# Kernel tuning notes

Hardware: AMD Instinct MI355X
Metric: run time of the kernel (lower is better)

## Reference

```python
import jax, jax.numpy as jnp
import numpy as np

N0, C1, C2 = 100000, 10000, 1000
E0 = 1_600_000
IN = 128
H = 128
OUT = 128


def _pool_edges(ei, ew, cluster, C):
    # PyG pool_edge: remap via cluster, drop self loops, coalesce (sum weights)
    m = cluster[ei]
    mask = m[0] != m[1]
    m = m[:, mask]
    w = ew[mask]
    keys = m[0] * C + m[1]
    uk, inv = np.unique(keys, return_inverse=True)
    w2 = np.bincount(inv, weights=w).astype(np.float32)
    return np.stack([uk // C, uk % C]).astype(np.int64), w2


def _with_self_loops(ei, ew, N):
    # gcn_norm(add_remaining_self_loops, fill_value=1); base edges have no loops
    row = np.concatenate([ei[0], np.arange(N)]).astype(np.int64)
    col = np.concatenate([ei[1], np.arange(N)]).astype(np.int64)
    w = np.concatenate([ew, np.ones(N, np.float32)])
    return row, col, w


def setup_inputs() -> dict:
    rng = np.random.default_rng(0)
    ei = rng.integers(0, N0, size=(2, E0))
    ei = ei[:, ei[0] != ei[1]]
    ew = np.ones(ei.shape[1], np.float32)
    # guaranteed-surjective cluster assignments (stand-in for Louvain output)
    c1 = rng.permutation(np.arange(N0) % C1).astype(np.int64)
    c2 = rng.permutation(np.arange(C1) % C2).astype(np.int64)
    ei1, ew1 = _pool_edges(ei, ew, c1, C1)
    ei2, ew2 = _pool_edges(ei1, ew1, c2, C2)
    r0, co0, w0 = _with_self_loops(ei, ew, N0)
    r1, co1, w1 = _with_self_loops(ei1, ew1, C1)
    r2, co2, w2 = _with_self_loops(ei2, ew2, C2)

    key = jax.random.key(0)
    ks = jax.random.split(key, 16)
    def lin(k, fi, fo):
        return jax.random.normal(k, (fi, fo), jnp.float32) / np.sqrt(fi)
    inp = {
        'x': jax.random.normal(ks[0], (N0, IN), jnp.float32),
        'W_pre': lin(ks[1], IN, H), 'b_pre': jnp.zeros((H,), jnp.float32),
        'W_u0': lin(ks[2], H, H), 'b_u0': jnp.zeros((H,), jnp.float32),
        'W_u1': lin(ks[3], H, H), 'b_u1': jnp.zeros((H,), jnp.float32),
        'W_u2': lin(ks[4], H, H), 'b_u2': jnp.zeros((H,), jnp.float32),
        'W_d0': lin(ks[5], H, OUT), 'b_d0': jnp.zeros((OUT,), jnp.float32),
        'W_d1': lin(ks[6], H, H), 'b_d1': jnp.zeros((H,), jnp.float32),
        'row0': jnp.asarray(r0), 'col0': jnp.asarray(co0), 'ew0': jnp.asarray(w0),
        'row1': jnp.asarray(r1), 'col1': jnp.asarray(co1), 'ew1': jnp.asarray(w1),
        'row2': jnp.asarray(r2), 'col2': jnp.asarray(co2), 'ew2': jnp.asarray(w2),
        'cluster1': jnp.asarray(c1), 'cluster2': jnp.asarray(c2),
    }
    return inp


def _gcn(x, W, b, row, col, ew, N):
    # PyG GCNConv: sym-normalized aggregation at target (col)
    deg = jax.ops.segment_sum(ew, col, num_segments=N)
    dinv = jnp.where(deg > 0, jax.lax.rsqrt(deg), 0.0)
    norm = dinv[row] * ew * dinv[col]
    h = x @ W                                   # [N, F_out]
    out = jax.ops.segment_sum(h[row] * norm[:, None], col, num_segments=N)
    return out + b


def _seg_mean(x, cluster, C):
    s = jax.ops.segment_sum(x, cluster, num_segments=C)
    cnt = jax.ops.segment_sum(jnp.ones((x.shape[0], 1), x.dtype), cluster,
                              num_segments=C)
    return s / jnp.maximum(cnt, 1.0)


def reference(x, W_pre, b_pre, W_u0, b_u0, W_u1, b_u1, W_u2, b_u2,
              W_d0, b_d0, W_d1, b_d1,
              row0, col0, ew0, row1, col1, ew1, row2, col2, ew2,
              cluster1, cluster2):
    # --- up (coarsening) path ---
    h = x @ W_pre + b_pre                                   # preembed
    x0 = jax.nn.relu(_gcn(h, W_u0, b_u0, row0, col0, ew0, N0))
    x1 = _seg_mean(x0, cluster1, C1)                        # avg_pool level 1
    x1 = jax.nn.relu(_gcn(x1, W_u1, b_u1, row1, col1, ew1, C1))
    x2 = _seg_mean(x1, cluster2, C2)                        # avg_pool level 2
    x2 = jax.nn.relu(_gcn(x2, W_u2, b_u2, row2, col2, ew2, C2))
    # --- down (unpooling) path; down convs use all-ones edge weights ---
    y = x1 + x2[cluster2]
    y = jax.nn.relu(_gcn(y, W_d1, b_d1, row1, col1, jnp.ones_like(ew1), C1))
    y = x0 + y[cluster1]
    y = _gcn(y, W_d0, b_d0, row0, col0, jnp.ones_like(ew0), N0)
    return y
```

## Files before the change

kernel.cpp:

```cpp
#include <hip/hip_runtime.h>

#define HH 128
static constexpr int kN0 = 100000;
static constexpr int kC1 = 10000;
static constexpr int kC2 = 1000;

static constexpr int B0 = kN0;
static constexpr int B1 = B0 + kC1;
static constexpr int B2 = B1 + kC2;
static constexpr int B3 = B2 + kC1;
static constexpr int NTOT = B3 + kC2;

static constexpr int NB0 = (kN0 + 127) / 128;
static constexpr int NB1 = (kC1 + 7) / 8;
static constexpr int NB2 = kC2;
static constexpr int NBP1 = (kC1 + 127) / 128;
static constexpr int NBP2 = (kC2 + 15) / 16;
static constexpr int Q0 = NB0;
static constexpr int Q1 = Q0 + NB1;
static constexpr int Q2 = Q1 + NB2;
static constexpr int Q3 = Q2 + NBP1;
static constexpr int NBK = Q3 + NBP2;

__device__ __forceinline__ int bucket_of(int bin) {
  if (bin < B0) return bin >> 7;
  if (bin < B1) return Q0 + ((bin - B0) >> 3);
  if (bin < B2) return Q1 + (bin - B1);
  if (bin < B3) return Q2 + ((bin - B2) >> 7);
  return Q3 + ((bin - B3) >> 4);
}

__device__ __forceinline__ unsigned int f2_to_bf2(float a, float b) {
  unsigned int ua = __float_as_uint(a);
  unsigned int ub = __float_as_uint(b);
  ua = (ua + 0x7fffu + ((ua >> 16) & 1u)) >> 16;
  ub = (ub + 0x7fffu + ((ub >> 16) & 1u)) & 0xffff0000u;
  return ua | ub;
}
__device__ __forceinline__ unsigned short f2bf(float f) {
  unsigned int u = __float_as_uint(f);
  u = (u + 0x7fffu + ((u >> 16) & 1u)) >> 16;
  return (unsigned short)u;
}
__device__ __forceinline__ float bf2f(unsigned short s) {
  return __uint_as_float(((unsigned int)s) << 16);
}

using bf16x8 = __attribute__((ext_vector_type(8))) short;
using f32x4 = __attribute__((ext_vector_type(4))) float;

__global__ __launch_bounds__(256) void p1_kernel(const int* __restrict__ col0,
                                                 const int* __restrict__ col1,
                                                 const int* __restrict__ col2,
                                                 const int* __restrict__ cl1,
                                                 const int* __restrict__ cl2,
                                                 int E0, int E1, int E2,
                                                 int* __restrict__ bucketCnt) {
  __shared__ int h[NBK];
  for (int i = threadIdx.x; i < NBK; i += 256) h[i] = 0;
  __syncthreads();
  int T0 = E0, T1 = T0 + E1, T2 = T1 + E2, T3 = T2 + kN0, T4 = T3 + kC1;
  for (int g = blockIdx.x * 256 + threadIdx.x; g < T4; g += gridDim.x * 256) {
    int bin;
    if (g < T0)      bin = col0[g];
    else if (g < T1) bin = B0 + col1[g - T0];
    else if (g < T2) bin = B1 + col2[g - T1];
    else if (g < T3) bin = B2 + cl1[g - T2];
    else             bin = B3 + cl2[g - T3];
    atomicAdd(&h[bucket_of(bin)], 1);
  }
  __syncthreads();
  for (int i = threadIdx.x; i < NBK; i += 256) {
    int c = h[i];
    if (c) atomicAdd(&bucketCnt[i], c);
  }
}

__global__ __launch_bounds__(1024) void p2_kernel(const int* __restrict__ bucketCnt,
                                                  int* __restrict__ bucketStart,
                                                  int* __restrict__ cursor,
                                                  int* __restrict__ startsg, int T) {
  int t = threadIdx.x;
  int v[4]; int s = 0;
#pragma unroll
  for (int j = 0; j < 4; j++) {
    int i = t * 4 + j;
    v[j] = (i < NBK) ? bucketCnt[i] : 0;
    s += v[j];
  }
  int lane = t & 63, w = t >> 6;
  int incl = s;
  for (int o = 1; o < 64; o <<= 1) { int u = __shfl_up(incl, o); if (lane >= o) incl += u; }
  __shared__ int wt[16];
  if (lane == 63) wt[w] = incl;
  __syncthreads();
  if (t == 0) { int run = 0; for (int i = 0; i < 16; i++) { int c = wt[i]; wt[i] = run; run += c; } }
  __syncthreads();
  int ex = wt[w] + incl - s;
#pragma unroll
  for (int j = 0; j < 4; j++) {
    int i = t * 4 + j;
    if (i < NBK) { bucketStart[i] = ex; cursor[i] = ex; }
    ex += v[j];
  }
  if (t == 0) { bucketStart[NBK] = T; startsg[NTOT] = T; }
}

__global__ __launch_bounds__(256) void p3_kernel(const int* __restrict__ col0,
                                                 const int* __restrict__ col1,
                                                 const int* __restrict__ col2,
                                                 const int* __restrict__ cl1,
                                                 const int* __restrict__ cl2,
                                                 const int* __restrict__ row0,
                                                 const int* __restrict__ row1,
                                                 const int* __restrict__ row2,
                                                 const float* __restrict__ ew1,
                                                 const float* __restrict__ ew2,
                                                 int E0, int E1, int E2,
                                                 int* __restrict__ cursor,
                                                 int4* __restrict__ part) {
  __shared__ int h[NBK];
  __shared__ int gbase[NBK];
  for (int i = threadIdx.x; i < NBK; i += 256) h[i] = 0;
  __syncthreads();
  int T0 = E0, T1 = T0 + E1, T2 = T1 + E2, T3 = T2 + kN0, T4 = T3 + kC1;
  int base = blockIdx.x * 4096;
  int bins[16], srcs[16], rk[16];
  float wv[16];
#pragma unroll
  for (int j = 0; j < 16; j++) {
    int g = base + threadIdx.x + j * 256;
    int bin = -1, src = 0; float w = 0.f;
    if (g < T4) {
      if (g < T0) { bin = col0[g]; src = row0[g]; }
      else if (g < T1) { int e = g - T0; bin = B0 + col1[e]; src = row1[e]; w = ew1[e]; }
      else if (g < T2) { int e = g - T1; bin = B1 + col2[e]; src = row2[e]; w = ew2[e]; }
      else if (g < T3) { int e = g - T2; bin = B2 + cl1[e]; src = e; }
      else             { int e = g - T3; bin = B3 + cl2[e]; src = e; }
    }
    bins[j] = bin; srcs[j] = src; wv[j] = w;
    rk[j] = (bin >= 0) ? atomicAdd(&h[bucket_of(bin)], 1) : 0;
  }
  __syncthreads();
  for (int i = threadIdx.x; i < NBK; i += 256) {
    int c = h[i];
    gbase[i] = c ? atomicAdd(&cursor[i], c) : 0;
  }
  __syncthreads();
#pragma unroll
  for (int j = 0; j < 16; j++) {
    if (bins[j] >= 0) {
      int slot = gbase[bucket_of(bins[j])] + rk[j];
      part[slot] = make_int4(bins[j], srcs[j], __float_as_int(wv[j]), 0);
    }
  }
}

__global__ __launch_bounds__(256) void p4_kernel(const int* __restrict__ bucketStart,
                                                 const int4* __restrict__ part,
                                                 int* __restrict__ startsg,
                                                 int* __restrict__ rowS,
                                                 float* __restrict__ ewSm) {
  int b = blockIdx.x;
  int binLo, width;
  if (b < Q0)      { binLo = b << 7;                 width = 128; if (binLo + width > B0) width = B0 - binLo; }
  else if (b < Q1) { binLo = B0 + ((b - Q0) << 3);   width = 8; }
  else if (b < Q2) { binLo = B1 + (b - Q1);          width = 1; }
  else if (b < Q3) { binLo = B2 + ((b - Q2) << 7);   width = 128; if (binLo + width > B3) width = B3 - binLo; }
  else             { binLo = B3 + ((b - Q3) << 4);   width = 16; if (binLo + width > NTOT) width = NTOT - binLo; }
  int base = bucketStart[b], nend = bucketStart[b + 1];
  int t = threadIdx.x;

  if (width == 1) {
    if (t == 0) startsg[binLo] = base;
    bool isEw = (binLo >= B0 && binLo < B2);
    for (int i = base + t; i < nend; i += 256) {
      int4 it = part[i];
      rowS[i] = it.y;
      if (isEw) ewSm[i] = __int_as_float(it.z);
    }
    return;
  }

  __shared__ int h[128];
  __shared__ int cur[128];
  if (t < 128) h[t] = 0;
  __syncthreads();
  for (int i = base + t; i < nend; i += 256) atomicAdd(&h[part[i].x - binLo], 1);
  __syncthreads();
  if (t == 0) {
    int run = 0;
    for (int j = 0; j < width; j++) {
      cur[j] = run;
      startsg[binLo + j] = base + run;
      run += h[j];
    }
  }
  __syncthreads();
  for (int i = base + t; i < nend; i += 256) {
    int4 it = part[i];
    int k = it.x;
    int r = atomicAdd(&cur[k - binLo], 1);
    int dst = base + r;
    rowS[dst] = it.y;
    if (k >= B0 && k < B2) ewSm[dst] = __int_as_float(it.z);
  }
}

__global__ void dinv_kernel(const int* __restrict__ startsg, const float* __restrict__ ewSm,
                            float* __restrict__ d0, float* __restrict__ d1w,
                            float* __restrict__ d1o, float* __restrict__ d2) {
  int t = blockIdx.x * 256 + threadIdx.x;
  if (t < kN0) {
    int c = startsg[t + 1] - startsg[t];
    d0[t] = c > 0 ? rsqrtf((float)c) : 0.f;
  }
  int wid = t >> 6, lane = t & 63;
  if (wid < kC1) {
    int s = startsg[B0 + wid], e = startsg[B0 + wid + 1];
    float a = 0.f;
    for (int k = s + lane; k < e; k += 64) a += ewSm[k];
    for (int o = 32; o > 0; o >>= 1) a += __shfl_down(a, o);
    if (lane == 0) {
      d1w[wid] = a > 0.f ? rsqrtf(a) : 0.f;
      int c = e - s;
      d1o[wid] = c > 0 ? rsqrtf((float)c) : 0.f;
    }
  } else if (wid < kC1 + kC2) {
    int w2 = wid - kC1;
    int s = startsg[B1 + w2], e = startsg[B1 + w2 + 1];
    float a = 0.f;
    for (int k = s + lane; k < e; k += 64) a += ewSm[k];
    for (int o = 32; o > 0; o >>= 1) a += __shfl_down(a, o);
    if (lane == 0) d2[w2] = a > 0.f ? rsqrtf(a) : 0.f;
  }
}

__global__ void wprep_kernel(const int* __restrict__ rowS, const float* __restrict__ ewSm,
                             const float* __restrict__ d1w, const float* __restrict__ d2,
                             int E0, int E1, int E2,
                             float* __restrict__ wAll) {
  int e = blockIdx.x * 256 + threadIdx.x + E0;
  int tot = E0 + E1 + E2;
  if (e >= tot) return;
  int r = rowS[e];
  if (e < E0 + E1) {
    wAll[e] = d1w[r] * ewSm[e];
  } else {
    wAll[e] = d2[r] * ewSm[e];
  }
}

__global__ __launch_bounds__(256) void matmul_kernel(const float* __restrict__ X,
                                                     const float* __restrict__ Xadd,
                                                     const int* __restrict__ cl,
                                                     const float* __restrict__ W,
                                                     const float* __restrict__ bias,
                                                     const float* __restrict__ rowScale,
                                                     float* __restrict__ Y,
                                                     unsigned int* __restrict__ Ybf, int N) {
  __shared__ float Ws[64 * 128];
  __shared__ float Xs[32 * 128];
  int t = threadIdx.x;
  int rbase = blockIdx.x * 32;
  const float4* X4 = (const float4*)X;
  float4* Xs4 = (float4*)Xs;
#pragma unroll
  for (int i = 0; i < 4; i++) {
    int idx = t + 256 * i;
    int fr = idx >> 5, fc = idx & 31;
    int row = rbase + fr; if (row >= N) row = N - 1;
    float4 v = X4[(size_t)row * 32 + fc];
    if (Xadd) {
      int c = cl[row];
      float4 u = ((const float4*)Xadd)[(size_t)c * 32 + fc];
      v.x += u.x; v.y += u.y; v.z += u.z; v.w += u.w;
    }
    Xs4[idx] = v;
  }
  float acc[4][4];
#pragma unroll
  for (int r = 0; r < 4; r++)
#pragma unroll
    for (int cc = 0; cc < 4; cc++) acc[r][cc] = 0.f;
  int c0 = (t & 31) * 4;
  int rl = (t >> 5) * 4;
  const float4* W4 = (const float4*)W;
  float4* Ws4 = (float4*)Ws;
  for (int half = 0; half < 2; half++) {
    __syncthreads();
#pragma unroll
    for (int i = 0; i < 8; i++) {
      int idx = t + 256 * i;
      Ws4[idx] = W4[half * 2048 + idx];
    }
    __syncthreads();
#pragma unroll 4
    for (int k = 0; k < 64; k++) {
      float4 w4 = *(const float4*)(Ws + k * 128 + c0);
      float xv[4];
#pragma unroll
      for (int r = 0; r < 4; r++) xv[r] = Xs[(rl + r) * 128 + half * 64 + k];
#pragma unroll
      for (int r = 0; r < 4; r++) {
        acc[r][0] = fmaf(xv[r], w4.x, acc[r][0]);
        acc[r][1] = fmaf(xv[r], w4.y, acc[r][1]);
        acc[r][2] = fmaf(xv[r], w4.z, acc[r][2]);
        acc[r][3] = fmaf(xv[r], w4.w, acc[r][3]);
      }
    }
  }
  float4 b4 = make_float4(0.f, 0.f, 0.f, 0.f);
  if (bias) b4 = *(const float4*)(bias + c0);
#pragma unroll
  for (int r = 0; r < 4; r++) {
    int row = rbase + rl + r;
    if (row < N) {
      float sc = rowScale ? rowScale[row] : 1.f;
      float4 o;
      o.x = (acc[r][0] + b4.x) * sc; o.y = (acc[r][1] + b4.y) * sc;
      o.z = (acc[r][2] + b4.z) * sc; o.w = (acc[r][3] + b4.w) * sc;
      if (Ybf) {
        unsigned int pk0 = f2_to_bf2(o.x, o.y);
        unsigned int pk1 = f2_to_bf2(o.z, o.w);
        *(uint2*)(Ybf + (size_t)row * 64 + (c0 >> 1)) = make_uint2(pk0, pk1);
      } else {
        *(float4*)(Y + (size_t)row * 128 + c0) = o;
      }
    }
  }
}

__global__ __launch_bounds__(256, 2) void mfma_gemm_kernel(
    const float* __restrict__ X, const float* __restrict__ Xadd,
    const int* __restrict__ cl, const float* __restrict__ W,
    const float* __restrict__ bias, const float* __restrict__ rowScale,
    unsigned int* __restrict__ Ybf, int N) {
  __shared__ unsigned int Bt[128 * 64];
  int t = threadIdx.x;
  {
    int n = t & 127, kh = t >> 7;
#pragma unroll
    for (int k = kh * 64; k < kh * 64 + 64; k += 2) {
      float a = W[(size_t)k * 128 + n];
      float b = W[(size_t)(k + 1) * 128 + n];
      unsigned int pk = (unsigned int)f2bf(a) | ((unsigned int)f2bf(b) << 16);
      unsigned int byteoff = ((unsigned int)(n * 256 + k * 2)) ^ (((unsigned int)n & 7u) << 4);
      *(unsigned int*)((char*)Bt + byteoff) = pk;
    }
  }
  __syncthreads();
  int wv = t >> 6, lane = t & 63;
  int g = lane >> 4, mrow = lane & 15;
  int rbase = blockIdx.x * 128 + wv * 32;
  bf16x8 ahi[2][4], alo[2][4];
#pragma unroll
  for (int mt = 0; mt < 2; mt++) {
    int row = rbase + mt * 16 + mrow;
    int rc = row < N ? row : N - 1;
    const float4* Xr = (const float4*)(X + (size_t)rc * 128);
    const float4* Ar = Xadd ? (const float4*)(Xadd + (size_t)cl[rc] * 128) : nullptr;
#pragma unroll
    for (int ks = 0; ks < 4; ks++) {
      int c4 = ks * 8 + g * 2;
      float4 v0 = Xr[c4], v1 = Xr[c4 + 1];
      if (Ar) {
        float4 u0 = Ar[c4], u1 = Ar[c4 + 1];
        v0.x += u0.x; v0.y += u0.y; v0.z += u0.z; v0.w += u0.w;
        v1.x += u1.x; v1.y += u1.y; v1.z += u1.z; v1.w += u1.w;
      }
      float vv[8] = {v0.x, v0.y, v0.z, v0.w, v1.x, v1.y, v1.z, v1.w};
      bf16x8 h, l;
#pragma unroll
      for (int j = 0; j < 8; j++) {
        unsigned short hb = f2bf(vv[j]);
        h[j] = (short)hb;
        l[j] = (short)f2bf(vv[j] - bf2f(hb));
      }
      ahi[mt][ks] = h; alo[mt][ks] = l;
    }
  }
  f32x4 acc[2][8];
#pragma unroll
  for (int mt = 0; mt < 2; mt++)
#pragma unroll
    for (int nt = 0; nt < 8; nt++) acc[mt][nt] = (f32x4){0.f, 0.f, 0.f, 0.f};
#pragma unroll
  for (int ks = 0; ks < 4; ks++) {
#pragma unroll
    for (int nt = 0; nt < 8; nt++) {
      int n = nt * 16 + mrow;
      unsigned int byteoff =
          ((unsigned int)(n * 256 + ks * 64 + g * 16)) ^ (((unsigned int)n & 7u) << 4);
      bf16x8 b = *(const bf16x8*)((const char*)Bt + byteoff);
      acc[0][nt] = __builtin_amdgcn_mfma_f32_16x16x32_bf16(ahi[0][ks], b, acc[0][nt], 0, 0, 0);
      acc[1][nt] = __builtin_amdgcn_mfma_f32_16x16x32_bf16(ahi[1][ks], b, acc[1][nt], 0, 0, 0);
      acc[0][nt] = __builtin_amdgcn_mfma_f32_16x16x32_bf16(alo[0][ks], b, acc[0][nt], 0, 0, 0);
      acc[1][nt] = __builtin_amdgcn_mfma_f32_16x16x32_bf16(alo[1][ks], b, acc[1][nt], 0, 0, 0);
    }
  }
#pragma unroll
  for (int mt = 0; mt < 2; mt++) {
#pragma unroll
    for (int r = 0; r < 4; r++) {
      int row = rbase + mt * 16 + g * 4 + r;
      if (row < N) {
        float sc = rowScale ? rowScale[row] : 1.f;
#pragma unroll
        for (int nt = 0; nt < 4; nt++) {
          int c = nt * 16 + mrow;
          float lo = (acc[mt][nt][r] + (bias ? bias[c] : 0.f)) * sc;
          float hi = (acc[mt][nt + 4][r] + (bias ? bias[c + 64] : 0.f)) * sc;
          Ybf[(size_t)row * 64 + c] = (unsigned int)f2bf(lo) | ((unsigned int)f2bf(hi) << 16);
        }
      }
    }
  }
}

__global__ __launch_bounds__(256) void agg_kernel(const unsigned int* __restrict__ Hf,
                                                  float* __restrict__ out,
                                                  const int* __restrict__ starts,
                                                  const int* __restrict__ rowS,
                                                  const float* __restrict__ dinv,
                                                  const float* __restrict__ bias,
                                                  int C, int relu) {
  int wid = (blockIdx.x * blockDim.x + threadIdx.x) >> 6;
  int lane = threadIdx.x & 63;
  if (wid >= C) return;
  int h = lane >> 5, hl = lane & 31;
  const uint2* Hf2 = (const uint2*)Hf;
  int s = starts[wid], e = starts[wid + 1];
  float dc = dinv[wid];
  float a0 = 0.f, a1 = 0.f, b0 = 0.f, b1 = 0.f;
  for (int base = s; base < e; base += 64) {
    int n = e - base; if (n > 64) n = 64;
    int r = rowS[base + (lane < n ? lane : 0)];
    for (int j = 0; j < n; j += 16) {
#pragma unroll
      for (int u = 0; u < 8; u++) {
        int eidx = j + u * 2 + h;
        bool v = eidx < n;
        int rr = __shfl(r, v ? eidx : 0);
        uint2 pv = Hf2[(size_t)rr * 32 + hl];
        if (!v) { pv.x = 0u; pv.y = 0u; }
        a0 += __uint_as_float(pv.x << 16);
        b0 += __uint_as_float(pv.x & 0xffff0000u);
        a1 += __uint_as_float(pv.y << 16);
        b1 += __uint_as_float(pv.y & 0xffff0000u);
      }
    }
  }
  a0 += __shfl_xor(a0, 32); a1 += __shfl_xor(a1, 32);
  b0 += __shfl_xor(b0, 32); b1 += __shfl_xor(b1, 32);
  int c0 = h * 64 + hl * 2;
  float o0 = (h ? b0 : a0) * dc + bias[c0];
  float o1 = (h ? b1 : a1) * dc + bias[c0 + 1];
  if (relu) { o0 = fmaxf(o0, 0.f); o1 = fmaxf(o1, 0.f); }
  *(float2*)(out + (size_t)wid * 128 + c0) = make_float2(o0, o1);
}

__global__ __launch_bounds__(256) void aggb_kernel(const unsigned int* __restrict__ Hf,
                                                   float* __restrict__ out,
                                                   const int* __restrict__ starts,
                                                   const int* __restrict__ rowS,
                                                   const float* __restrict__ wS,
                                                   const float* __restrict__ dinv,
                                                   const float* __restrict__ bias,
                                                   int C, int relu) {
  int node = blockIdx.x;
  if (node >= C) return;
  int wv = threadIdx.x >> 6, lane = threadIdx.x & 63;
  int h = lane >> 5, hl = lane & 31;
  const uint2* Hf2 = (const uint2*)Hf;
  int s = starts[node], e = starts[node + 1];
  float a0 = 0.f, a1 = 0.f, a2 = 0.f, a3 = 0.f;
  for (int base = s + wv * 64; base < e; base += 256) {
    int n = e - base; if (n > 64) n = 64;
    int moff = base + (lane < n ? lane : 0);
    int r = rowS[moff];
    float w = wS[moff];
    for (int j = 0; j < n; j += 16) {
#pragma unroll
      for (int u = 0; u < 8; u++) {
        int eidx = j + u * 2 + h;
        bool v = eidx < n;
        int rr = __shfl(r, v ? eidx : 0);
        float ww = __shfl(w, v ? eidx : 0);
        if (!v) ww = 0.f;
        uint2 pv = Hf2[(size_t)rr * 32 + hl];
        a0 = fmaf(ww, __uint_as_float(pv.x << 16), a0);
        a1 = fmaf(ww, __uint_as_float(pv.x & 0xffff0000u), a1);
        a2 = fmaf(ww, __uint_as_float(pv.y << 16), a2);
        a3 = fmaf(ww, __uint_as_float(pv.y & 0xffff0000u), a3);
      }
    }
  }
  a0 += __shfl_xor(a0, 32); a1 += __shfl_xor(a1, 32);
  a2 += __shfl_xor(a2, 32); a3 += __shfl_xor(a3, 32);
  __shared__ float4 sh[4][32];
  if (h == 0) sh[wv][hl] = make_float4(a0, a1, a2, a3);
  __syncthreads();
  if (threadIdx.x < 32) {
    float4 v0 = sh[0][threadIdx.x], v1 = sh[1][threadIdx.x];
    float4 v2 = sh[2][threadIdx.x], v3 = sh[3][threadIdx.x];
    float dc = dinv[node];
    int c0 = threadIdx.x * 4;
    float4 bb = *(const float4*)(bias + c0);
    float4 o;
    o.x = (v0.x + v1.x + v2.x + v3.x) * dc + bb.x;
    o.y = (v0.y + v1.y + v2.y + v3.y) * dc + bb.y;
    o.z = (v0.z + v1.z + v2.z + v3.z) * dc + bb.z;
    o.w = (v0.w + v1.w + v2.w + v3.w) * dc + bb.w;
    if (relu) {
      o.x = fmaxf(o.x, 0.f); o.y = fmaxf(o.y, 0.f);
      o.z = fmaxf(o.z, 0.f); o.w = fmaxf(o.w, 0.f);
    }
    *(float4*)(out + (size_t)node * 128 + c0) = o;
  }
}

__global__ __launch_bounds__(256) void aggb1_kernel(const unsigned int* __restrict__ Hf,
                                                    float* __restrict__ out,
                                                    const int* __restrict__ starts,
                                                    const int* __restrict__ rowS,
                                                    const float* __restrict__ dinv,
                                                    const float* __restrict__ bias,
                                                    int C, int relu) {
  int node = blockIdx.x;
  if (node >= C) return;
  int wv = threadIdx.x >> 6, lane = threadIdx.x & 63;
  int h = lane >> 5, hl = lane & 31;
  const uint2* Hf2 = (const uint2*)Hf;
  int s = starts[node], e = starts[node + 1];
  float a0 = 0.f, a1 = 0.f, a2 = 0.f, a3 = 0.f;
  for (int base = s + wv * 64; base < e; base += 256) {
    int n = e - base; if (n > 64) n = 64;
    int r = rowS[base + (lane < n ? lane : 0)];
    for (int j = 0; j < n; j += 16) {
#pragma unroll
      for (int u = 0; u < 8; u++) {
        int eidx = j + u * 2 + h;
        bool v = eidx < n;
        int rr = __shfl(r, v ? eidx : 0);
        uint2 pv = Hf2[(size_t)rr * 32 + hl];
        if (!v) { pv.x = 0u; pv.y = 0u; }
        a0 += __uint_as_float(pv.x << 16);
        a1 += __uint_as_float(pv.x & 0xffff0000u);
        a2 += __uint_as_float(pv.y << 16);
        a3 += __uint_as_float(pv.y & 0xffff0000u);
      }
    }
  }
  a0 += __shfl_xor(a0, 32); a1 += __shfl_xor(a1, 32);
  a2 += __shfl_xor(a2, 32); a3 += __shfl_xor(a3, 32);
  __shared__ float4 sh[4][32];
  if (h == 0) sh[wv][hl] = make_float4(a0, a1, a2, a3);
  __syncthreads();
  if (threadIdx.x < 32) {
    float4 v0 = sh[0][threadIdx.x], v1 = sh[1][threadIdx.x];
    float4 v2 = sh[2][threadIdx.x], v3 = sh[3][threadIdx.x];
    float dc = dinv[node];
    int c0 = threadIdx.x * 4;
    float4 bb = *(const float4*)(bias + c0);
    float4 o;
    o.x = (v0.x + v1.x + v2.x + v3.x) * dc + bb.x;
    o.y = (v0.y + v1.y + v2.y + v3.y) * dc + bb.y;
    o.z = (v0.z + v1.z + v2.z + v3.z) * dc + bb.z;
    o.w = (v0.w + v1.w + v2.w + v3.w) * dc + bb.w;
    if (relu) {
      o.x = fmaxf(o.x, 0.f); o.y = fmaxf(o.y, 0.f);
      o.z = fmaxf(o.z, 0.f); o.w = fmaxf(o.w, 0.f);
    }
    *(float4*)(out + (size_t)node * 128 + c0) = o;
  }
}

__global__ __launch_bounds__(256) void pool_kernel(const float* __restrict__ src,
                                                   float* __restrict__ out,
                                                   const int* __restrict__ starts,
                                                   const int* __restrict__ rowS, int C) {
  int wid = (blockIdx.x * blockDim.x + threadIdx.x) >> 6;
  int lane = threadIdx.x & 63;
  if (wid >= C) return;
  int s = starts[wid], e = starts[wid + 1];
  float ax0 = 0.f, ay0 = 0.f, ax1 = 0.f, ay1 = 0.f;
  int m = s;
  for (; m + 7 < e; m += 8) {
    int idx[8];
#pragma unroll
    for (int u = 0; u < 8; u++) idx[u] = rowS[m + u];
#pragma unroll
    for (int u = 0; u < 8; u++) {
      float2 v = *(const float2*)(src + (size_t)idx[u] * 128 + lane * 2);
      if (u & 1) { ax1 += v.x; ay1 += v.y; } else { ax0 += v.x; ay0 += v.y; }
    }
  }
  for (; m < e; m++) {
    int id = rowS[m];
    const float2 v = *(const float2*)(src + (size_t)id * 128 + lane * 2);
    ax0 += v.x; ay0 += v.y;
  }
  float inv = (e > s) ? 1.f / (float)(e - s) : 0.f;
  *(float2*)(out + (size_t)wid * 128 + lane * 2) =
      make_float2((ax0 + ax1) * inv, (ay0 + ay1) * inv);
}


extern "C" void kernel_launch(void* const* d_in, const int* in_sizes, int n_in,
                              void* d_out, int out_size, void* d_ws, size_t ws_size,
                              hipStream_t stream) {
  const float* x     = (const float*)d_in[0];
  const float* W_pre = (const float*)d_in[1];
  const float* b_pre = (const float*)d_in[2];
  const float* W_u0  = (const float*)d_in[3];
  const float* b_u0  = (const float*)d_in[4];
  const float* W_u1  = (const float*)d_in[5];
  const float* b_u1  = (const float*)d_in[6];
  const float* W_u2  = (const float*)d_in[7];
  const float* b_u2  = (const float*)d_in[8];
  const float* W_d0  = (const float*)d_in[9];
  const float* b_d0  = (const float*)d_in[10];
  const float* W_d1  = (const float*)d_in[11];
  const float* b_d1  = (const float*)d_in[12];
  const int* row0 = (const int*)d_in[13];
  const int* col0 = (const int*)d_in[14];
  const int* row1 = (const int*)d_in[16];
  const int* col1 = (const int*)d_in[17];
  const float* ew1 = (const float*)d_in[18];
  const int* row2 = (const int*)d_in[19];
  const int* col2 = (const int*)d_in[20];
  const float* ew2 = (const float*)d_in[21];
  const int* cluster1 = (const int*)d_in[22];
  const int* cluster2 = (const int*)d_in[23];
  int E0 = in_sizes[13], E1 = in_sizes[16], E2 = in_sizes[19];
  float* out = (float*)d_out;
  int Ttot = E0 + E1 + E2 + kN0 + kC1;
  int Etot = E0 + E1 + E2;

  char* basep = (char*)d_ws;
  size_t off = 0;
  auto alloc = [&](size_t bytes) -> char* {
    char* p = basep + off;
    off = (off + bytes + 255) & ~(size_t)255;
    return p;
  };
  int* bucketCnt = (int*)alloc((size_t)NBK * 4);
  size_t zero_bytes = off;
  int* bucketStart = (int*)alloc((size_t)(NBK + 1) * 4);
  int* cursor      = (int*)alloc((size_t)NBK * 4);
  int* startsg     = (int*)alloc((size_t)(NTOT + 1) * 4);
  int* rowS  = (int*)alloc((size_t)Ttot * 4);
  float* ewS = (float*)alloc((size_t)(E1 + E2) * 4);
  float* ewSm = ewS - E0;
  float* dinv0  = (float*)alloc((size_t)kN0 * 4);
  float* dinv1w = (float*)alloc((size_t)kC1 * 4);
  float* dinv1o = (float*)alloc((size_t)kC1 * 4);
  float* dinv2  = (float*)alloc((size_t)kC2 * 4);
  size_t watermark = off;
  int4* part = (int4*)alloc((size_t)Ttot * 16);
  off = watermark;
  float* wAll = (float*)alloc((size_t)Etot * 4);
  float* Wf   = (float*)alloc((size_t)128 * 128 * 4);
  float* bfv  = (float*)alloc((size_t)128 * 4);
  float* A    = (float*)alloc((size_t)kN0 * HH * 4);
  float* s1a  = (float*)alloc((size_t)kC1 * HH * 4);
  float* s1b  = (float*)alloc((size_t)kC1 * HH * 4);
  float* s2a  = (float*)alloc((size_t)kC2 * HH * 4);
  unsigned int* s1bb = (unsigned int*)alloc((size_t)kC1 * 64 * 4);
  unsigned int* s2bb = (unsigned int*)alloc((size_t)kC2 * 64 * 4);
  unsigned int* s1cb = (unsigned int*)alloc((size_t)kC1 * 64 * 4);
  unsigned int* tb   = (unsigned int*)alloc((size_t)kN0 * 64 * 4);
  unsigned int* t0   = (unsigned int*)d_out;

  hipMemsetAsync(d_ws, 0, zero_bytes, stream);

  auto cdiv = [](int a, int b) { return (a + b - 1) / b; };

  p1_kernel<<<256, 256, 0, stream>>>(col0, col1, col2, cluster1, cluster2, E0, E1, E2, bucketCnt);
  p2_kernel<<<1, 1024, 0, stream>>>(bucketCnt, bucketStart, cursor, startsg, Ttot);
  p3_kernel<<<cdiv(Ttot, 4096), 256, 0, stream>>>(col0, col1, col2, cluster1, cluster2,
                                                  row0, row1, row2, ew1, ew2, E0, E1, E2,
                                                  cursor, part);
  p4_kernel<<<NBK, 256, 0, stream>>>(bucketStart, part, startsg, rowS, ewSm);
  dinv_kernel<<<cdiv((kC1 + kC2) * 64, 256), 256, 0, stream>>>(startsg, ewSm, dinv0, dinv1w,
                                                               dinv1o, dinv2);
  wprep_kernel<<<cdiv(E1 + E2, 256), 256, 0, stream>>>(rowS, ewSm, dinv1w, dinv2,
                                                       E0, E1, E2, wAll);

  matmul_kernel<<<cdiv(128, 32), 256, 0, stream>>>(W_pre, nullptr, nullptr, W_u0, nullptr,
                                                   nullptr, Wf, nullptr, 128);
  matmul_kernel<<<1, 256, 0, stream>>>(b_pre, nullptr, nullptr, W_u0, nullptr,
                                       nullptr, bfv, nullptr, 1);
  mfma_gemm_kernel<<<cdiv(kN0, 128), 256, 0, stream>>>(x, nullptr, nullptr, Wf, bfv, dinv0,
                                                       t0, kN0);
  agg_kernel<<<cdiv(kN0, 4), 256, 0, stream>>>(t0, A, startsg, rowS, dinv0, b_u0, kN0, 1);
  pool_kernel<<<cdiv(kC1, 4), 256, 0, stream>>>(A, s1a, startsg + B2, rowS, kC1);
  matmul_kernel<<<cdiv(kC1, 32), 256, 0, stream>>>(s1a, nullptr, nullptr, W_u1, nullptr,
                                                   nullptr, nullptr, s1bb, kC1);
  aggb_kernel<<<kC1, 256, 0, stream>>>(s1bb, s1a, startsg + B0, rowS, wAll, dinv1w, b_u1, kC1, 1);
  pool_kernel<<<cdiv(kC2, 4), 256, 0, stream>>>(s1a, s2a, startsg + B3, rowS, kC2);
  matmul_kernel<<<cdiv(kC2, 32), 256, 0, stream>>>(s2a, nullptr, nullptr, W_u2, nullptr,
                                                   nullptr, nullptr, s2bb, kC2);
  aggb_kernel<<<kC2, 256, 0, stream>>>(s2bb, s2a, startsg + B1, rowS, wAll, dinv2, b_u2, kC2, 1);
  matmul_kernel<<<cdiv(kC1, 32), 256, 0, stream>>>(s1a, s2a, cluster2, W_d1, nullptr,
                                                   dinv1o, nullptr, s1cb, kC1);
  aggb1_kernel<<<kC1, 256, 0, stream>>>(s1cb, s1b, startsg + B0, rowS, dinv1o, b_d1, kC1, 1);
  mfma_gemm_kernel<<<cdiv(kN0, 128), 256, 0, stream>>>(A, s1b, cluster1, W_d0, nullptr, dinv0,
                                                       tb, kN0);
  agg_kernel<<<cdiv(kN0, 4), 256, 0, stream>>>(tb, out, startsg, rowS, dinv0, b_d0, kN0, 0);
}
```

Measured before the change: 634.6 us.

## Partition scatter kernel with few large chunks and two-pass histogram

The bucket-scatter kernel now launches 128 blocks, each covering a large contiguous chunk of edges, in place of one block per 4096 edges. Each block makes a histogram pass over its chunk, reserves global ranges once per bucket, then re-reads the edges and scatters using shared-memory atomics as local cursors. This cuts the number of global cursor atomics and per-block bucket reservations, at the cost of reading the column arrays twice and running far fewer blocks. Slots within a bucket are now assigned in nondeterministic order within each block.

```diff
diff --git a/kernel.cpp b/kernel.cpp
--- a/kernel.cpp
+++ b/kernel.cpp
@@ -21,6 +21,8 @@
 static constexpr int Q2 = Q1 + NB2;
 static constexpr int Q3 = Q2 + NBP1;
 static constexpr int NBK = Q3 + NBP2;
+
+static constexpr int P3_BLOCKS = 128;
 
 __device__ __forceinline__ int bucket_of(int bin) {
   if (bin < B0) return bin >> 7;
@@ -120,39 +122,36 @@
                                                  int* __restrict__ cursor,
                                                  int4* __restrict__ part) {
   __shared__ int h[NBK];
-  __shared__ int gbase[NBK];
   for (int i = threadIdx.x; i < NBK; i += 256) h[i] = 0;
   __syncthreads();
   int T0 = E0, T1 = T0 + E1, T2 = T1 + E2, T3 = T2 + kN0, T4 = T3 + kC1;
-  int base = blockIdx.x * 4096;
-  int bins[16], srcs[16], rk[16];
-  float wv[16];
-#pragma unroll
-  for (int j = 0; j < 16; j++) {
-    int g = base + threadIdx.x + j * 256;
-    int bin = -1, src = 0; float w = 0.f;
-    if (g < T4) {
-      if (g < T0) { bin = col0[g]; src = row0[g]; }
-      else if (g < T1) { int e = g - T0; bin = B0 + col1[e]; src = row1[e]; w = ew1[e]; }
-      else if (g < T2) { int e = g - T1; bin = B1 + col2[e]; src = row2[e]; w = ew2[e]; }
-      else if (g < T3) { int e = g - T2; bin = B2 + cl1[e]; src = e; }
-      else             { int e = g - T3; bin = B3 + cl2[e]; src = e; }
-    }
-    bins[j] = bin; srcs[j] = src; wv[j] = w;
-    rk[j] = (bin >= 0) ? atomicAdd(&h[bucket_of(bin)], 1) : 0;
+  int chunk = ((T4 + P3_BLOCKS - 1) / P3_BLOCKS + 255) & ~255;
+  int start = blockIdx.x * chunk;
+  int end = start + chunk; if (end > T4) end = T4;
+  for (int g = start + (int)threadIdx.x; g < end; g += 256) {
+    int bin;
+    if (g < T0)      bin = col0[g];
+    else if (g < T1) bin = B0 + col1[g - T0];
+    else if (g < T2) bin = B1 + col2[g - T1];
+    else if (g < T3) bin = B2 + cl1[g - T2];
+    else             bin = B3 + cl2[g - T3];
+    atomicAdd(&h[bucket_of(bin)], 1);
   }
   __syncthreads();
   for (int i = threadIdx.x; i < NBK; i += 256) {
     int c = h[i];
-    gbase[i] = c ? atomicAdd(&cursor[i], c) : 0;
-  }
-  __syncthreads();
-#pragma unroll
-  for (int j = 0; j < 16; j++) {
-    if (bins[j] >= 0) {
-      int slot = gbase[bucket_of(bins[j])] + rk[j];
-      part[slot] = make_int4(bins[j], srcs[j], __float_as_int(wv[j]), 0);
-    }
+    h[i] = c ? atomicAdd(&cursor[i], c) : 0;
+  }
+  __syncthreads();
+  for (int g = start + (int)threadIdx.x; g < end; g += 256) {
+    int bin, src; float w = 0.f;
+    if (g < T0)      { bin = col0[g]; src = row0[g]; }
+    else if (g < T1) { int e = g - T0; bin = B0 + col1[e]; src = row1[e]; w = ew1[e]; }
+    else if (g < T2) { int e = g - T1; bin = B1 + col2[e]; src = row2[e]; w = ew2[e]; }
+    else if (g < T3) { int e = g - T2; bin = B2 + cl1[e]; src = e; }
+    else             { int e = g - T3; bin = B3 + cl2[e]; src = e; }
+    int slot = atomicAdd(&h[bucket_of(bin)], 1);
+    part[slot] = make_int4(bin, src, __float_as_int(w), 0);
   }
 }
 
@@ -679,9 +678,9 @@
 
   p1_kernel<<<256, 256, 0, stream>>>(col0, col1, col2, cluster1, cluster2, E0, E1, E2, bucketCnt);
   p2_kernel<<<1, 1024, 0, stream>>>(bucketCnt, bucketStart, cursor, startsg, Ttot);
-  p3_kernel<<<cdiv(Ttot, 4096), 256, 0, stream>>>(col0, col1, col2, cluster1, cluster2,
-                                                  row0, row1, row2, ew1, ew2, E0, E1, E2,
-                                                  cursor, part);
+  p3_kernel<<<P3_BLOCKS, 256, 0, stream>>>(col0, col1, col2, cluster1, cluster2,
+                                           row0, row1, row2, ew1, ew2, E0, E1, E2,
+                                           cursor, part);
   p4_kernel<<<NBK, 256, 0, stream>>>(bucketStart, part, startsg, rowS, ewSm);
   dinv_kernel<<<cdiv((kC1 + kC2) * 64, 256), 256, 0, stream>>>(startsg, ewSm, dinv0, dinv1w,
                                                                dinv1o, dinv2);
```

Measured after the change: 787.8 us. +24.1%, slower.
